# Kernel tuning notes

Hardware: AMD Instinct MI355X
Metric: run time of the kernel (lower is better)

The kernel has to match this reference:

```python
import jax, jax.numpy as jnp
import numpy as np

BZ, N_STEPS, D_IN, D_HID, D_OUT = 4096, 128, 32, 128, 32


def setup_inputs() -> dict:
    key = jax.random.key(0)
    ks = jax.random.split(key, 16)
    g = lambda k, s: jax.random.normal(k, s, dtype=jnp.float32) * 0.05
    return {
        "fcn_latent": g(ks[0], (BZ, D_IN)),
        "encoder_outputs": g(ks[1], (BZ, N_STEPS, D_HID)),
        "att1_w": g(ks[2], (D_IN, 2 * D_IN)),
        "att1_b": g(ks[3], (D_IN,)),
        "att2_w": g(ks[4], (D_HID, 2 * D_HID)),
        "att2_b": g(ks[5], (D_HID,)),
        "gru1_wih": g(ks[6], (3 * D_HID, D_IN)),
        "gru1_whh": g(ks[7], (3 * D_HID, D_HID)),
        "gru1_bih": g(ks[8], (3 * D_HID,)),
        "gru1_bhh": g(ks[9], (3 * D_HID,)),
        "gru2_wih": g(ks[10], (3 * D_HID, D_HID)),
        "gru2_whh": g(ks[11], (3 * D_HID, D_HID)),
        "gru2_bih": g(ks[12], (3 * D_HID,)),
        "gru2_bhh": g(ks[13], (3 * D_HID,)),
        "out_w": g(ks[14], (D_OUT, D_HID)),
        "out_b": g(ks[15], (D_OUT,)),
    }


def _gru_cell(x, h, w_ih, w_hh, b_ih, b_hh):
    # torch.nn.GRUCell math: gates ordered (r, z, n)
    gi = x @ w_ih.T + b_ih
    gh = h @ w_hh.T + b_hh
    i_r, i_z, i_n = jnp.split(gi, 3, axis=-1)
    h_r, h_z, h_n = jnp.split(gh, 3, axis=-1)
    r = jax.nn.sigmoid(i_r + h_r)
    z = jax.nn.sigmoid(i_z + h_z)
    n = jnp.tanh(i_n + r * h_n)
    return (1.0 - z) * n + z * h


def _attend(h, enc_t, w, b):
    # h: (bz, D), enc_t: (bz, d_enc). Faithful to original (mixes batch into contraction).
    scores = h.T @ enc_t                     # (D, d_enc)
    weight = jax.nn.softmax(scores, axis=-1)
    context = (weight @ enc_t.T).T           # (bz, D)
    return jnp.tanh(jnp.concatenate([context, h], axis=1) @ w.T + b)


def reference(fcn_latent, encoder_outputs, att1_w, att1_b, att2_w, att2_b,
              gru1_wih, gru1_whh, gru1_bih, gru1_bhh,
              gru2_wih, gru2_whh, gru2_bih, gru2_bhh, out_w, out_b):
    # step 0: attention over d_input-sized hidden, then GRUCell(d_input -> d_hidden)
    att0 = _attend(fcn_latent, encoder_outputs[:, 0, :], att1_w, att1_b)
    h_rep = jnp.tile(fcn_latent, (1, D_HID // D_IN))          # (bz, d_hidden)
    h = _gru_cell(att0, h_rep, gru1_wih, gru1_whh, gru1_bih, gru1_bhh)

    def step(h, enc_t):
        a = _attend(h, enc_t, att2_w, att2_b)
        h2 = _gru_cell(a, h, gru2_wih, gru2_whh, gru2_bih, gru2_bhh)
        return h2, h2

    enc_rest = jnp.swapaxes(encoder_outputs[:, 1:, :], 0, 1)  # (n_steps-1, bz, d_hidden)
    _, hs_rest = jax.lax.scan(step, h, enc_rest)
    collector = jnp.concatenate([h[:, None, :], jnp.swapaxes(hs_rest, 0, 1)], axis=1)
    reconstruction = collector @ out_w.T + out_b              # (bz, n_steps, d_output)
    return reconstruction
```

## Files before the change

### kernel.cpp

```cpp
#include <hip/hip_runtime.h>
#include <math.h>

#define BZ 4096
#define NT 128
#define DH 128
#define DI 32
#define LDW 132
#define SCR_KS 2116
#define SA 136
#define ST 40

typedef short bf16x8 __attribute__((ext_vector_type(8)));
typedef float f32x4 __attribute__((ext_vector_type(4)));

__device__ __forceinline__ float4 ld4(const float* p) { return *(const float4*)(p); }
__device__ __forceinline__ void st4(float* p, float4 v) { *(float4*)(p) = v; }
__device__ __forceinline__ float dot4(float4 w, float4 a) {
  return w.x*a.x + w.y*a.y + w.z*a.z + w.w*a.w;
}
__device__ __forceinline__ float sigm(float x) { return 1.f / (1.f + expf(-x)); }
__device__ __forceinline__ unsigned short f2b(float x) {
  unsigned u = __float_as_uint(x);
  u += 0x7FFFu + ((u >> 16) & 1u);
  return (unsigned short)(u >> 16);
}

__global__ __launch_bounds__(512) void k_prep(const float* __restrict__ a2w,
                                              const float* __restrict__ wih,
                                              const float* __restrict__ whh,
                                              const float* __restrict__ outw,
                                              unsigned short* __restrict__ wbf) {
  const int idx = blockIdx.x * 512 + threadIdx.x;
  if (idx >= 147456) return;
  const int tile = idx >> 14, pos = idx & 16383;
  float v;
  if (tile == 0)      v = a2w[(pos >> 7) * 256 + (pos & 127)];
  else if (tile == 1) v = a2w[(pos >> 7) * 256 + 128 + (pos & 127)];
  else if (tile == 2) v = wih[pos];
  else if (tile == 3) v = whh[pos];
  else if (tile == 4) v = wih[16384 + pos];
  else if (tile == 5) v = whh[16384 + pos];
  else if (tile == 6) v = wih[32768 + pos];
  else if (tile == 7) v = whh[32768 + pos];
  else                v = (pos < 4096) ? outw[pos] : 0.f;
  wbf[idx] = f2b(v);
}

template<int D>
__global__ __launch_bounds__(512) void k_scores(const float* __restrict__ hsrc,
                                                const float* __restrict__ enc,
                                                int t, float* __restrict__ spart) {
  constexpr int IG = D / 8;
  constexpr int JC = (D == 128) ? 4 : 1;
  constexpr int HS = D + 4;
  __shared__ float hs[64 * HS];
  __shared__ float es[64 * LDW];
  const int p = blockIdx.x, tid = threadIdx.x, b0 = p * 64;
  for (int idx = tid; idx < 64 * (D / 4); idx += 512) {
    const int r = idx / (D / 4), c4 = (idx % (D / 4)) * 4;
    st4(hs + r * HS + c4, ld4(hsrc + (size_t)(b0 + r) * D + c4));
  }
  for (int idx = tid; idx < 64 * 32; idx += 512) {
    const int r = idx >> 5, c4 = (idx & 31) << 2;
    st4(es + r * LDW + c4, ld4(enc + ((size_t)(b0 + r) * NT + t) * DH + c4));
  }
  __syncthreads();
  const int ig = tid % IG, jg = tid / IG;
  const int i0 = ig * 8, j0 = jg * JC;
  float acc[8][JC];
#pragma unroll
  for (int a = 0; a < 8; ++a)
#pragma unroll
    for (int b = 0; b < JC; ++b) acc[a][b] = 0.f;
  for (int b = 0; b < 64; ++b) {
    float4 h0 = ld4(hs + b * HS + i0);
    float4 h1 = ld4(hs + b * HS + i0 + 4);
    float hv[8] = {h0.x, h0.y, h0.z, h0.w, h1.x, h1.y, h1.z, h1.w};
    float ev[JC];
    if (JC == 4) {
      float4 e = ld4(es + b * LDW + j0);
      ev[0] = e.x; ev[1] = e.y; ev[2] = e.z; ev[3] = e.w;
    } else {
      ev[0] = es[b * LDW + j0];
    }
#pragma unroll
    for (int ii = 0; ii < 8; ++ii)
#pragma unroll
      for (int jj = 0; jj < JC; ++jj) acc[ii][jj] += hv[ii] * ev[jj];
  }
#pragma unroll
  for (int ii = 0; ii < 8; ++ii)
#pragma unroll
    for (int jj = 0; jj < JC; ++jj)
      spart[((size_t)p * D + (i0 + ii)) * 128 + j0 + jj] = acc[ii][jj];
}

template<int R, int P>
__global__ __launch_bounds__(128) void k_soft(const float* __restrict__ spart,
                                              float* __restrict__ W,
                                              unsigned short* __restrict__ Wmb) {
  const int r = blockIdx.x, j = threadIdx.x;
  float s = 0.f;
#pragma unroll 8
  for (int p = 0; p < P; ++p) s += spart[((size_t)p * R + r) * 128 + j];
  __shared__ float xm[2], xs[2];
  float m = s;
  for (int o = 1; o < 64; o <<= 1) m = fmaxf(m, __shfl_xor(m, o));
  if ((j & 63) == 0) xm[j >> 6] = m;
  __syncthreads();
  m = fmaxf(xm[0], xm[1]);
  float e = expf(s - m);
  float sum = e;
  for (int o = 1; o < 64; o <<= 1) sum += __shfl_xor(sum, o);
  if ((j & 63) == 0) xs[j >> 6] = sum;
  __syncthreads();
  sum = xs[0] + xs[1];
  const float val = e / sum;
  W[r * 128 + j] = val;
  Wmb[r * 128 + j] = f2b(val);
}

__global__ __launch_bounds__(512) void k_soft2(const float* __restrict__ spart,
                                               unsigned short* __restrict__ Wmb) {
  __shared__ float scr[512];
  __shared__ float xred[4];
  const int r = blockIdx.x, tid = threadIdx.x;
  const int j = tid & 127, pc = tid >> 7;
  float s = 0.f;
#pragma unroll 8
  for (int p = pc * 32; p < (pc + 1) * 32; ++p)
    s += spart[((size_t)p * 128 + r) * 128 + j];
  scr[pc * 128 + j] = s;
  __syncthreads();
  if (tid < 128) {
    const float sv = scr[tid] + scr[128 + tid] + scr[256 + tid] + scr[384 + tid];
    float m = sv;
    for (int o = 1; o < 64; o <<= 1) m = fmaxf(m, __shfl_xor(m, o));
    if ((tid & 63) == 0) xred[tid >> 6] = m;
  }
  __syncthreads();
  if (tid < 128) {
    const float sv = scr[tid] + scr[128 + tid] + scr[256 + tid] + scr[384 + tid];
    const float m = fmaxf(xred[0], xred[1]);
    float ev = expf(sv - m);
    float sum = ev;
    for (int o = 1; o < 64; o <<= 1) sum += __shfl_xor(sum, o);
    if ((tid & 63) == 0) xred[2 + (tid >> 6)] = sum;
  }
  __syncthreads();
  if (tid < 128) {
    const float sv = scr[tid] + scr[128 + tid] + scr[256 + tid] + scr[384 + tid];
    const float m = fmaxf(xred[0], xred[1]);
    const float sum = xred[2] + xred[3];
    Wmb[r * 128 + tid] = f2b(expf(sv - m) / sum);
  }
}

struct WTile { bf16x8 k[4]; };
struct AFrag { bf16x8 k[4]; };

__device__ __forceinline__ void loadW(WTile& wt, const unsigned short* __restrict__ base,
                                      int R, int g) {
#pragma unroll
  for (int ks = 0; ks < 4; ++ks)
    wt.k[ks] = *(const bf16x8*)(base + (size_t)R * 128 + ks * 32 + g * 8);
}
__device__ __forceinline__ void loadA(AFrag& a, const unsigned short* act, int n, int g) {
  const char* ab = (const char*)act + n * (2 * SA) + g * 16;
#pragma unroll
  for (int ks = 0; ks < 4; ++ks) a.k[ks] = *(const bf16x8*)(ab + ks * 64);
}
__device__ __forceinline__ void mmrr(f32x4& acc, const AFrag& a, const WTile& w) {
#pragma unroll
  for (int ks = 0; ks < 4; ++ks)
    acc = __builtin_amdgcn_mfma_f32_16x16x32_bf16(a.k[ks], w.k[ks], acc, 0, 0, 0);
}

__global__ __launch_bounds__(512, 2) void k_step2(
    const float* __restrict__ enc, int t, int do_next,
    const unsigned short* __restrict__ Wmb, const unsigned short* __restrict__ wbf,
    const float* __restrict__ att2b,
    const float* __restrict__ bih, const float* __restrict__ bhh,
    const float* __restrict__ outb,
    float* __restrict__ h, float* __restrict__ out, float* __restrict__ spart) {
  __shared__ __align__(16) unsigned short el[32 * SA], hl[32 * SA];
  __shared__ __align__(16) unsigned short ctxl[32 * SA], al[32 * SA], hnl[32 * SA];
  __shared__ __align__(16) unsigned short hnT[128 * ST], encT[128 * ST];
  const int tid = threadIdx.x, b0 = blockIdx.x * 32;
  const int w = tid >> 6, l = tid & 63;
  const int n = l & 15, g4 = l >> 4;
  const int c = w * 16 + n;
  const f32x4 z4 = {0.f, 0.f, 0.f, 0.f};

  WTile wWm, wA2a, wA2b, wIR, wHR, wIZ, wHZ, wIN, wHN;
  loadW(wWm, Wmb, c, g4);
  loadW(wA2a, wbf + 0 * 16384, c, g4);
  loadW(wA2b, wbf + 1 * 16384, c, g4);
  loadW(wIR,  wbf + 2 * 16384, c, g4);
  loadW(wHR,  wbf + 3 * 16384, c, g4);
  loadW(wIZ,  wbf + 4 * 16384, c, g4);
  loadW(wHZ,  wbf + 5 * 16384, c, g4);
  loadW(wIN,  wbf + 6 * 16384, c, g4);
  loadW(wHN,  wbf + 7 * 16384, c, g4);

  {
    const int r = tid >> 4, c8 = (tid & 15) << 3;
    float4 e0 = ld4(enc + ((size_t)(b0 + r) * NT + t) * DH + c8);
    float4 e1 = ld4(enc + ((size_t)(b0 + r) * NT + t) * DH + c8 + 4);
    float4 h0 = ld4(h + (size_t)(b0 + r) * DH + c8);
    float4 h1 = ld4(h + (size_t)(b0 + r) * DH + c8 + 4);
    unsigned short* ep = el + r * SA + c8;
    ep[0]=f2b(e0.x); ep[1]=f2b(e0.y); ep[2]=f2b(e0.z); ep[3]=f2b(e0.w);
    ep[4]=f2b(e1.x); ep[5]=f2b(e1.y); ep[6]=f2b(e1.z); ep[7]=f2b(e1.w);
    unsigned short* hp = hl + r * SA + c8;
    hp[0]=f2b(h0.x); hp[1]=f2b(h0.y); hp[2]=f2b(h0.z); hp[3]=f2b(h0.w);
    hp[4]=f2b(h1.x); hp[5]=f2b(h1.y); hp[6]=f2b(h1.z); hp[7]=f2b(h1.w);
  }
  if (do_next) {
    const int r = tid & 31, c8 = (tid >> 5) << 3;
    float4 e0 = ld4(enc + ((size_t)(b0 + r) * NT + t + 1) * DH + c8);
    float4 e1 = ld4(enc + ((size_t)(b0 + r) * NT + t + 1) * DH + c8 + 4);
    encT[(c8 + 0) * ST + r] = f2b(e0.x); encT[(c8 + 1) * ST + r] = f2b(e0.y);
    encT[(c8 + 2) * ST + r] = f2b(e0.z); encT[(c8 + 3) * ST + r] = f2b(e0.w);
    encT[(c8 + 4) * ST + r] = f2b(e1.x); encT[(c8 + 5) * ST + r] = f2b(e1.y);
    encT[(c8 + 6) * ST + r] = f2b(e1.z); encT[(c8 + 7) * ST + r] = f2b(e1.w);
  }
  float hprev[2][4];
#pragma unroll
  for (int hh = 0; hh < 2; ++hh)
#pragma unroll
    for (int j = 0; j < 4; ++j)
      hprev[hh][j] = h[(size_t)(b0 + hh * 16 + g4 * 4 + j) * DH + c];
  const float b2c = att2b[c];
  const float bihR = bih[c], bihZ = bih[DH + c], bihN = bih[2 * DH + c];
  const float bhhR = bhh[c], bhhZ = bhh[DH + c], bhhN = bhh[2 * DH + c];
  __syncthreads();

#pragma unroll
  for (int hh = 0; hh < 2; ++hh) {
    AFrag fE;
    loadA(fE, el + hh * 16 * SA, n, g4);
    f32x4 aC = z4;
    mmrr(aC, fE, wWm);
#pragma unroll
    for (int j = 0; j < 4; ++j) ctxl[(hh * 16 + g4 * 4 + j) * SA + c] = f2b(aC[j]);
  }
  __syncthreads();
#pragma unroll
  for (int hh = 0; hh < 2; ++hh) {
    AFrag fC, fH;
    loadA(fC, ctxl + hh * 16 * SA, n, g4);
    loadA(fH, hl + hh * 16 * SA, n, g4);
    f32x4 aA = z4;
    mmrr(aA, fC, wA2a);
    mmrr(aA, fH, wA2b);
#pragma unroll
    for (int j = 0; j < 4; ++j)
      al[(hh * 16 + g4 * 4 + j) * SA + c] = f2b(tanhf(aA[j] + b2c));
  }
  __syncthreads();
  f32x4 aR[2], aZ[2], aIN[2], aHN[2];
#pragma unroll
  for (int hh = 0; hh < 2; ++hh) {
    AFrag fA, fH;
    loadA(fA, al + hh * 16 * SA, n, g4);
    loadA(fH, hl + hh * 16 * SA, n, g4);
    f32x4 tr_ = z4, tz = z4, ti = z4, th = z4;
    mmrr(tr_, fA, wIR); mmrr(tr_, fH, wHR);
    mmrr(tz, fA, wIZ);  mmrr(tz, fH, wHZ);
    mmrr(ti, fA, wIN);  mmrr(th, fH, wHN);
    aR[hh] = tr_; aZ[hh] = tz; aIN[hh] = ti; aHN[hh] = th;
  }
#pragma unroll
  for (int hh = 0; hh < 2; ++hh) {
#pragma unroll
    for (int j = 0; j < 4; ++j) {
      const int row = hh * 16 + g4 * 4 + j;
      const float rg = sigm(aR[hh][j] + bihR + bhhR);
      const float zg = sigm(aZ[hh][j] + bihZ + bhhZ);
      const float ng = tanhf(aIN[hh][j] + bihN + rg * (aHN[hh][j] + bhhN));
      const float hv = (1.f - zg) * ng + zg * hprev[hh][j];
      const unsigned short hb = f2b(hv);
      hnl[row * SA + c] = hb;
      hnT[c * ST + row] = hb;
      h[(size_t)(b0 + row) * DH + c] = hv;
    }
  }
  __syncthreads();
  if (w < 2) {
    WTile wOut;
    loadW(wOut, wbf + 8 * 16384, c, g4);
    const float ob = outb[c];
#pragma unroll
    for (int hh = 0; hh < 2; ++hh) {
      AFrag fO;
      loadA(fO, hnl + hh * 16 * SA, n, g4);
      f32x4 o = z4;
      mmrr(o, fO, wOut);
#pragma unroll
      for (int j = 0; j < 4; ++j)
        out[((size_t)(b0 + hh * 16 + g4 * 4 + j) * NT + t) * DI + c] = o[j] + ob;
    }
  }
  if (do_next) {
    bf16x8 afr = *(const bf16x8*)(hnT + (16 * w + n) * ST + g4 * 8);
    float* spb = spart + ((size_t)blockIdx.x * 128 + 16 * w + g4 * 4) * 128 + n;
#pragma unroll
    for (int nt = 0; nt < 8; ++nt) {
      bf16x8 bfr = *(const bf16x8*)(encT + (16 * nt + n) * ST + g4 * 8);
      f32x4 s = __builtin_amdgcn_mfma_f32_16x16x32_bf16(afr, bfr, z4, 0, 0, 0);
#pragma unroll
      for (int jj = 0; jj < 4; ++jj) spb[(size_t)jj * 128 + 16 * nt] = s[jj];
    }
  }
}

__device__ __forceinline__ void stage128(float* dst, const float* __restrict__ src,
                                         int rows, int srcStride, int tid) {
  const int n4 = rows * 32;
  for (int idx = tid; idx < n4; idx += 512) {
    const int r = idx >> 5, c4 = (idx & 31) << 2;
    st4(dst + r * LDW + c4, ld4(src + (size_t)r * srcStride + c4));
  }
}
template<int ADD>
__device__ __forceinline__ void phase128(float* Wb, const float* act, float* dest, int tid) {
  const int ks = tid & 7, cg_ = (tid >> 3) & 15, r4 = tid >> 7;
  const int rbase = r4 * 4;
  float acc[4][8];
#pragma unroll
  for (int a = 0; a < 4; ++a)
#pragma unroll
    for (int b = 0; b < 8; ++b) acc[a][b] = 0.f;
#pragma unroll
  for (int ch = 0; ch < 4; ++ch) {
    const int k = ks * 4 + ch * 32;
    float4 av[4];
#pragma unroll
    for (int ri = 0; ri < 4; ++ri) av[ri] = ld4(act + (rbase + ri) * LDW + k);
#pragma unroll
    for (int i = 0; i < 8; ++i) {
      float4 wv = ld4(Wb + (cg_ * 8 + i) * LDW + k);
#pragma unroll
      for (int ri = 0; ri < 4; ++ri) acc[ri][i] += dot4(wv, av[ri]);
    }
  }
  __syncthreads();
#pragma unroll
  for (int ri = 0; ri < 4; ++ri) {
    st4(Wb + ks * SCR_KS + (rbase + ri) * LDW + cg_ * 8,
        make_float4(acc[ri][0], acc[ri][1], acc[ri][2], acc[ri][3]));
    st4(Wb + ks * SCR_KS + (rbase + ri) * LDW + cg_ * 8 + 4,
        make_float4(acc[ri][4], acc[ri][5], acc[ri][6], acc[ri][7]));
  }
  __syncthreads();
  const int fr = tid >> 5, fc = (tid & 31) << 2;
  float4 s = make_float4(0.f, 0.f, 0.f, 0.f);
#pragma unroll
  for (int kk = 0; kk < 8; ++kk) {
    float4 v = ld4(Wb + kk * SCR_KS + fr * LDW + fc);
    s.x += v.x; s.y += v.y; s.z += v.z; s.w += v.w;
  }
  float* dp = dest + fr * LDW + fc;
  if (ADD) { float4 o = ld4(dp); s.x += o.x; s.y += o.y; s.z += o.z; s.w += o.w; }
  st4(dp, s);
  __syncthreads();
}
__device__ __forceinline__ void gru_out(float p0, float p1, float p2, float p3,
                                        float bi0, float bi1, float bi2,
                                        float bh0, float bh1, float bh2,
                                        float hv, float* o) {
  const float rg = sigm(p0 + bi0 + bh0);
  const float zg = sigm(p1 + bi1 + bh1);
  const float ng = tanhf(p2 + bi2 + rg * (p3 + bh2));
  *o = (1.f - zg) * ng + zg * hv;
}
__global__ __launch_bounds__(512) void k_main0(
    const float* __restrict__ enc, const float* __restrict__ fcn,
    const float* __restrict__ W0,
    const float* __restrict__ A1, const float* __restrict__ b1,
    const float* __restrict__ wih, const float* __restrict__ whh,
    const float* __restrict__ bih, const float* __restrict__ bhh,
    const float* __restrict__ outw, const float* __restrict__ outb,
    float* __restrict__ h, float* __restrict__ out) {
  __shared__ float Wb[16960];
  __shared__ float el[16 * LDW], hrep[16 * LDW], al[16 * LDW], hn[16 * LDW];
  __shared__ float pre[4][16 * LDW];
  __shared__ float fl[16 * 36];
  const int tid = threadIdx.x, b0 = blockIdx.x * 16;
  {
    const int r = tid >> 5, c4 = (tid & 31) << 2;
    st4(el + r * LDW + c4, ld4(enc + ((size_t)(b0 + r) * NT + 0) * DH + c4));
  }
  {
    const int r = tid >> 5, cc = tid & 31;
    fl[r * 36 + cc] = fcn[(size_t)(b0 + r) * DI + cc];
  }
  __syncthreads();
  {
    const int r = tid >> 5, fc = (tid & 31) << 2;
    st4(hrep + r * LDW + fc, ld4(fl + r * 36 + (fc & 31)));
  }
  stage128(Wb, W0, 32, 128, tid);
  __syncthreads();
  {
    const int r = tid >> 5, q = tid & 31;
    float acc = 0.f;
#pragma unroll 8
    for (int k4 = 0; k4 < 32; ++k4)
      acc += dot4(ld4(Wb + q * LDW + k4 * 4), ld4(el + r * LDW + k4 * 4));
    hn[r * LDW + q] = acc;
  }
  __syncthreads();
  for (int idx = tid; idx < 512; idx += 512) {
    const int r = idx >> 4, c4 = (idx & 15) << 2;
    st4(Wb + r * 68 + c4, ld4(A1 + r * 64 + c4));
  }
  __syncthreads();
  {
    const int r = tid >> 5, i = tid & 31;
    float acc = b1[i];
#pragma unroll
    for (int k4 = 0; k4 < 8; ++k4)
      acc += dot4(ld4(Wb + i * 68 + k4 * 4), ld4(hn + r * LDW + k4 * 4));
#pragma unroll
    for (int k4 = 0; k4 < 8; ++k4)
      acc += dot4(ld4(Wb + i * 68 + 32 + k4 * 4), ld4(fl + r * 36 + k4 * 4));
    al[r * LDW + i] = tanhf(acc);
  }
  __syncthreads();
  for (int idx = tid; idx < 384 * 8; idx += 512) {
    const int r = idx >> 3, c4 = (idx & 7) << 2;
    st4(Wb + r * 36 + c4, ld4(wih + r * 32 + c4));
  }
  __syncthreads();
  {
    const int r = tid >> 5, ccc = tid & 31;
#pragma unroll
    for (int m = 0; m < 12; ++m) {
      const int cc = ccc + 32 * m, g = cc >> 7, col = cc & 127;
      float acc = 0.f;
#pragma unroll
      for (int k4 = 0; k4 < 8; ++k4)
        acc += dot4(ld4(Wb + cc * 36 + k4 * 4), ld4(al + r * LDW + k4 * 4));
      pre[(g == 2) ? 2 : g][r * LDW + col] = acc;
    }
  }
  __syncthreads();
  stage128(Wb, whh, 128, 128, tid);          __syncthreads();
  phase128<1>(Wb, hrep, pre[0], tid);
  stage128(Wb, whh + 16384, 128, 128, tid);  __syncthreads();
  phase128<1>(Wb, hrep, pre[1], tid);
  stage128(Wb, whh + 32768, 128, 128, tid);  __syncthreads();
  phase128<0>(Wb, hrep, pre[3], tid);
  {
    const int fr = tid >> 5, fc = (tid & 31) << 2;
    float4 p0 = ld4(&pre[0][fr * LDW + fc]), p1 = ld4(&pre[1][fr * LDW + fc]);
    float4 p2 = ld4(&pre[2][fr * LDW + fc]), p3 = ld4(&pre[3][fr * LDW + fc]);
    float4 bi0 = ld4(bih + fc), bi1 = ld4(bih + DH + fc), bi2 = ld4(bih + 2 * DH + fc);
    float4 bh0 = ld4(bhh + fc), bh1 = ld4(bhh + DH + fc), bh2 = ld4(bhh + 2 * DH + fc);
    float4 hv = ld4(hrep + fr * LDW + fc);
    float o0, o1, o2, o3;
    gru_out(p0.x, p1.x, p2.x, p3.x, bi0.x, bi1.x, bi2.x, bh0.x, bh1.x, bh2.x, hv.x, &o0);
    gru_out(p0.y, p1.y, p2.y, p3.y, bi0.y, bi1.y, bi2.y, bh0.y, bh1.y, bh2.y, hv.y, &o1);
    gru_out(p0.z, p1.z, p2.z, p3.z, bi0.z, bi1.z, bi2.z, bh0.z, bh1.z, bh2.z, hv.z, &o2);
    gru_out(p0.w, p1.w, p2.w, p3.w, bi0.w, bi1.w, bi2.w, bh0.w, bh1.w, bh2.w, hv.w, &o3);
    float4 hnew = make_float4(o0, o1, o2, o3);
    st4(hn + fr * LDW + fc, hnew);
    st4(h + (size_t)(b0 + fr) * DH + fc, hnew);
  }
  __syncthreads();
  stage128(Wb, outw, 32, 128, tid);
  __syncthreads();
  {
    const int r = tid >> 5, cc = tid & 31;
    float acc = outb[cc];
#pragma unroll 8
    for (int k4 = 0; k4 < 32; ++k4)
      acc += dot4(ld4(Wb + cc * LDW + k4 * 4), ld4(hn + r * LDW + k4 * 4));
    out[((size_t)(b0 + r) * NT + 0) * DI + cc] = acc;
  }
}

extern "C" void kernel_launch(void* const* d_in, const int* in_sizes, int n_in,
                              void* d_out, int out_size, void* d_ws, size_t ws_size,
                              hipStream_t stream) {
  (void)in_sizes; (void)n_in; (void)out_size; (void)ws_size;
  const float* fcn  = (const float*)d_in[0];
  const float* enc  = (const float*)d_in[1];
  const float* a1w  = (const float*)d_in[2];
  const float* a1b  = (const float*)d_in[3];
  const float* a2w  = (const float*)d_in[4];
  const float* a2b  = (const float*)d_in[5];
  const float* w1ih = (const float*)d_in[6];
  const float* w1hh = (const float*)d_in[7];
  const float* b1ih = (const float*)d_in[8];
  const float* b1hh = (const float*)d_in[9];
  const float* w2ih = (const float*)d_in[10];
  const float* w2hh = (const float*)d_in[11];
  const float* b2ih = (const float*)d_in[12];
  const float* b2hh = (const float*)d_in[13];
  const float* outw = (const float*)d_in[14];
  const float* outb = (const float*)d_in[15];
  float* out = (float*)d_out;
  float* ws  = (float*)d_ws;

  float* h     = ws;
  float* spart = ws + 524288;
  float* Wbuf  = ws + 2621440;
  unsigned short* wbf = (unsigned short*)(ws + 2637824);
  unsigned short* Wmb = (unsigned short*)(ws + 2712576);

  k_prep<<<288, 512, 0, stream>>>(a2w, w2ih, w2hh, outw, wbf);

  k_scores<DI><<<64, 512, 0, stream>>>(fcn, enc, 0, spart);
  k_soft<DI, 64><<<DI, 128, 0, stream>>>(spart, Wbuf, Wmb);
  k_main0<<<BZ / 16, 512, 0, stream>>>(enc, fcn, Wbuf, a1w, a1b,
                                       w1ih, w1hh, b1ih, b1hh, outw, outb, h, out);
  k_scores<DH><<<64, 512, 0, stream>>>(h, enc, 1, spart);
  k_soft<DH, 64><<<DH, 128, 0, stream>>>(spart, Wbuf, Wmb);

  for (int t = 1; t < NT; ++t) {
    const int do_next = (t < NT - 1) ? 1 : 0;
    k_step2<<<128, 512, 0, stream>>>(enc, t, do_next, Wmb, wbf, a2b,
                                     b2ih, b2hh, outb, h, out, spart);
    if (do_next)
      k_soft2<<<128, 512, 0, stream>>>(spart, Wmb);
  }
}
```

Before: 3.338 ms.

## Fuse score reduction and softmax into step kernel via atomic accumulation

Drops the separate per-step softmax kernel. Each step block now accumulates its partial attention scores straight into a shared global buffer with atomicAdd, and at the start of the next step recomputes the softmax redundantly per block into a swizzled LDS slot. A ring of four score buffers is rotated, with one buffer zeroed ahead of use, which removes one kernel launch and the partial-score round trip per step. In exchange the atomics contend on a 128x128 buffer, every block repeats the softmax work, and float atomic ordering makes the results nondeterministic.

```diff
diff --git a/kernel.cpp b/kernel.cpp
--- a/kernel.cpp
+++ b/kernel.cpp
@@ -120,40 +120,15 @@
   Wmb[r * 128 + j] = f2b(val);
 }
 
-__global__ __launch_bounds__(512) void k_soft2(const float* __restrict__ spart,
-                                               unsigned short* __restrict__ Wmb) {
-  __shared__ float scr[512];
-  __shared__ float xred[4];
-  const int r = blockIdx.x, tid = threadIdx.x;
-  const int j = tid & 127, pc = tid >> 7;
+__global__ __launch_bounds__(128) void k_sum(const float* __restrict__ spart,
+                                             float* __restrict__ S1,
+                                             float* __restrict__ S2) {
+  const int r = blockIdx.x, j = threadIdx.x;
   float s = 0.f;
 #pragma unroll 8
-  for (int p = pc * 32; p < (pc + 1) * 32; ++p)
-    s += spart[((size_t)p * 128 + r) * 128 + j];
-  scr[pc * 128 + j] = s;
-  __syncthreads();
-  if (tid < 128) {
-    const float sv = scr[tid] + scr[128 + tid] + scr[256 + tid] + scr[384 + tid];
-    float m = sv;
-    for (int o = 1; o < 64; o <<= 1) m = fmaxf(m, __shfl_xor(m, o));
-    if ((tid & 63) == 0) xred[tid >> 6] = m;
-  }
-  __syncthreads();
-  if (tid < 128) {
-    const float sv = scr[tid] + scr[128 + tid] + scr[256 + tid] + scr[384 + tid];
-    const float m = fmaxf(xred[0], xred[1]);
-    float ev = expf(sv - m);
-    float sum = ev;
-    for (int o = 1; o < 64; o <<= 1) sum += __shfl_xor(sum, o);
-    if ((tid & 63) == 0) xred[2 + (tid >> 6)] = sum;
-  }
-  __syncthreads();
-  if (tid < 128) {
-    const float sv = scr[tid] + scr[128 + tid] + scr[256 + tid] + scr[384 + tid];
-    const float m = fmaxf(xred[0], xred[1]);
-    const float sum = xred[2] + xred[3];
-    Wmb[r * 128 + tid] = f2b(expf(sv - m) / sum);
-  }
+  for (int p = 0; p < 64; ++p) s += spart[((size_t)p * 128 + r) * 128 + j];
+  S1[r * 128 + j] = s;
+  S2[r * 128 + j] = 0.f;
 }
 
 struct WTile { bf16x8 k[4]; };
@@ -175,14 +150,28 @@
   for (int ks = 0; ks < 4; ++ks)
     acc = __builtin_amdgcn_mfma_f32_16x16x32_bf16(a.k[ks], w.k[ks], acc, 0, 0, 0);
 }
-
-__global__ __launch_bounds__(512, 2) void k_step2(
+__device__ __forceinline__ void mmls(f32x4& acc, const unsigned short* Wt,
+                                     const unsigned short* act, int R, int n, int g) {
+  const char* ab = (const char*)act + n * (2 * SA) + g * 16;
+  const char* wb = (const char*)Wt;
+  const int sw = (R & 7) << 4;
+#pragma unroll
+  for (int ks = 0; ks < 4; ++ks) {
+    bf16x8 b = *(const bf16x8*)(wb + ((R * 256 + ks * 64 + g * 16) ^ sw));
+    bf16x8 a = *(const bf16x8*)(ab + ks * 64);
+    acc = __builtin_amdgcn_mfma_f32_16x16x32_bf16(a, b, acc, 0, 0, 0);
+  }
+}
+
+__global__ __launch_bounds__(512, 2) void k_step3(
     const float* __restrict__ enc, int t, int do_next,
-    const unsigned short* __restrict__ Wmb, const unsigned short* __restrict__ wbf,
+    const float* __restrict__ Srd, float* __restrict__ Sac, float* __restrict__ Szr,
+    const unsigned short* __restrict__ wbf,
     const float* __restrict__ att2b,
     const float* __restrict__ bih, const float* __restrict__ bhh,
     const float* __restrict__ outb,
-    float* __restrict__ h, float* __restrict__ out, float* __restrict__ spart) {
+    float* __restrict__ h, float* __restrict__ out) {
+  __shared__ __align__(16) unsigned short Wslot[16384];
   __shared__ __align__(16) unsigned short el[32 * SA], hl[32 * SA];
   __shared__ __align__(16) unsigned short ctxl[32 * SA], al[32 * SA], hnl[32 * SA];
   __shared__ __align__(16) unsigned short hnT[128 * ST], encT[128 * ST];
@@ -192,8 +181,67 @@
   const int c = w * 16 + n;
   const f32x4 z4 = {0.f, 0.f, 0.f, 0.f};
 
-  WTile wWm, wA2a, wA2b, wIR, wHR, wIZ, wHZ, wIN, wHN;
-  loadW(wWm, Wmb, c, g4);
+  {
+    const int row = tid >> 2, q = tid & 3;
+    const float* sr = Srd + row * 128 + q * 32;
+    float4 v[8];
+    float mx = -1e30f;
+#pragma unroll
+    for (int i = 0; i < 8; ++i) {
+      v[i] = ld4(sr + 4 * i);
+      mx = fmaxf(mx, fmaxf(fmaxf(v[i].x, v[i].y), fmaxf(v[i].z, v[i].w)));
+    }
+    mx = fmaxf(mx, __shfl_xor(mx, 1));
+    mx = fmaxf(mx, __shfl_xor(mx, 2));
+    float sum = 0.f;
+#pragma unroll
+    for (int i = 0; i < 8; ++i) {
+      v[i].x = expf(v[i].x - mx); v[i].y = expf(v[i].y - mx);
+      v[i].z = expf(v[i].z - mx); v[i].w = expf(v[i].w - mx);
+      sum += (v[i].x + v[i].y) + (v[i].z + v[i].w);
+    }
+    sum += __shfl_xor(sum, 1);
+    sum += __shfl_xor(sum, 2);
+    const float inv = 1.f / sum;
+    char* wb = (char*)Wslot;
+    const int sw = (row & 7) << 4;
+#pragma unroll
+    for (int ch = 0; ch < 4; ++ch) {
+      unsigned short h8[8] = {
+        f2b(v[2*ch].x * inv),   f2b(v[2*ch].y * inv),
+        f2b(v[2*ch].z * inv),   f2b(v[2*ch].w * inv),
+        f2b(v[2*ch+1].x * inv), f2b(v[2*ch+1].y * inv),
+        f2b(v[2*ch+1].z * inv), f2b(v[2*ch+1].w * inv)
+      };
+      *(uint4*)(wb + ((row * 256 + q * 64 + ch * 16) ^ sw)) = *(const uint4*)h8;
+    }
+  }
+
+  {
+    const int r = tid >> 4, c8 = (tid & 15) << 3;
+    float4 e0 = ld4(enc + ((size_t)(b0 + r) * NT + t) * DH + c8);
+    float4 e1 = ld4(enc + ((size_t)(b0 + r) * NT + t) * DH + c8 + 4);
+    float4 h0 = ld4(h + (size_t)(b0 + r) * DH + c8);
+    float4 h1 = ld4(h + (size_t)(b0 + r) * DH + c8 + 4);
+    unsigned short e8[8] = {f2b(e0.x), f2b(e0.y), f2b(e0.z), f2b(e0.w),
+                            f2b(e1.x), f2b(e1.y), f2b(e1.z), f2b(e1.w)};
+    unsigned short h8[8] = {f2b(h0.x), f2b(h0.y), f2b(h0.z), f2b(h0.w),
+                            f2b(h1.x), f2b(h1.y), f2b(h1.z), f2b(h1.w)};
+    *(uint4*)(el + r * SA + c8) = *(const uint4*)e8;
+    *(uint4*)(hl + r * SA + c8) = *(const uint4*)h8;
+  }
+  if (do_next) {
+    const int r = tid & 31, c8 = (tid >> 5) << 3;
+    float4 e0 = ld4(enc + ((size_t)(b0 + r) * NT + t + 1) * DH + c8);
+    float4 e1 = ld4(enc + ((size_t)(b0 + r) * NT + t + 1) * DH + c8 + 4);
+    encT[(c8 + 0) * ST + r] = f2b(e0.x); encT[(c8 + 1) * ST + r] = f2b(e0.y);
+    encT[(c8 + 2) * ST + r] = f2b(e0.z); encT[(c8 + 3) * ST + r] = f2b(e0.w);
+    encT[(c8 + 4) * ST + r] = f2b(e1.x); encT[(c8 + 5) * ST + r] = f2b(e1.y);
+    encT[(c8 + 6) * ST + r] = f2b(e1.z); encT[(c8 + 7) * ST + r] = f2b(e1.w);
+  }
+  if (do_next && tid < 128) Szr[blockIdx.x * 128 + tid] = 0.f;
+
+  WTile wA2a, wA2b, wIR, wHR, wIZ, wHZ, wIN, wHN;
   loadW(wA2a, wbf + 0 * 16384, c, g4);
   loadW(wA2b, wbf + 1 * 16384, c, g4);
   loadW(wIR,  wbf + 2 * 16384, c, g4);
@@ -203,28 +251,6 @@
   loadW(wIN,  wbf + 6 * 16384, c, g4);
   loadW(wHN,  wbf + 7 * 16384, c, g4);
 
-  {
-    const int r = tid >> 4, c8 = (tid & 15) << 3;
-    float4 e0 = ld4(enc + ((size_t)(b0 + r) * NT + t) * DH + c8);
-    float4 e1 = ld4(enc + ((size_t)(b0 + r) * NT + t) * DH + c8 + 4);
-    float4 h0 = ld4(h + (size_t)(b0 + r) * DH + c8);
-    float4 h1 = ld4(h + (size_t)(b0 + r) * DH + c8 + 4);
-    unsigned short* ep = el + r * SA + c8;
-    ep[0]=f2b(e0.x); ep[1]=f2b(e0.y); ep[2]=f2b(e0.z); ep[3]=f2b(e0.w);
-    ep[4]=f2b(e1.x); ep[5]=f2b(e1.y); ep[6]=f2b(e1.z); ep[7]=f2b(e1.w);
-    unsigned short* hp = hl + r * SA + c8;
-    hp[0]=f2b(h0.x); hp[1]=f2b(h0.y); hp[2]=f2b(h0.z); hp[3]=f2b(h0.w);
-    hp[4]=f2b(h1.x); hp[5]=f2b(h1.y); hp[6]=f2b(h1.z); hp[7]=f2b(h1.w);
-  }
-  if (do_next) {
-    const int r = tid & 31, c8 = (tid >> 5) << 3;
-    float4 e0 = ld4(enc + ((size_t)(b0 + r) * NT + t + 1) * DH + c8);
-    float4 e1 = ld4(enc + ((size_t)(b0 + r) * NT + t + 1) * DH + c8 + 4);
-    encT[(c8 + 0) * ST + r] = f2b(e0.x); encT[(c8 + 1) * ST + r] = f2b(e0.y);
-    encT[(c8 + 2) * ST + r] = f2b(e0.z); encT[(c8 + 3) * ST + r] = f2b(e0.w);
-    encT[(c8 + 4) * ST + r] = f2b(e1.x); encT[(c8 + 5) * ST + r] = f2b(e1.y);
-    encT[(c8 + 6) * ST + r] = f2b(e1.z); encT[(c8 + 7) * ST + r] = f2b(e1.w);
-  }
   float hprev[2][4];
 #pragma unroll
   for (int hh = 0; hh < 2; ++hh)
@@ -238,10 +264,8 @@
 
 #pragma unroll
   for (int hh = 0; hh < 2; ++hh) {
-    AFrag fE;
-    loadA(fE, el + hh * 16 * SA, n, g4);
     f32x4 aC = z4;
-    mmrr(aC, fE, wWm);
+    mmls(aC, Wslot, el + hh * 16 * SA, c, n, g4);
 #pragma unroll
     for (int j = 0; j < 4; ++j) ctxl[(hh * 16 + g4 * 4 + j) * SA + c] = f2b(aC[j]);
   }
@@ -304,13 +328,13 @@
   }
   if (do_next) {
     bf16x8 afr = *(const bf16x8*)(hnT + (16 * w + n) * ST + g4 * 8);
-    float* spb = spart + ((size_t)blockIdx.x * 128 + 16 * w + g4 * 4) * 128 + n;
+    float* Sn = Sac + (size_t)(16 * w + g4 * 4) * 128 + n;
 #pragma unroll
     for (int nt = 0; nt < 8; ++nt) {
       bf16x8 bfr = *(const bf16x8*)(encT + (16 * nt + n) * ST + g4 * 8);
       f32x4 s = __builtin_amdgcn_mfma_f32_16x16x32_bf16(afr, bfr, z4, 0, 0, 0);
 #pragma unroll
-      for (int jj = 0; jj < 4; ++jj) spb[(size_t)jj * 128 + 16 * nt] = s[jj];
+      for (int jj = 0; jj < 4; ++jj) atomicAdd(Sn + jj * 128 + nt * 16, s[jj]);
     }
   }
 }
@@ -507,9 +531,10 @@
 
   float* h     = ws;
   float* spart = ws + 524288;
-  float* Wbuf  = ws + 2621440;
-  unsigned short* wbf = (unsigned short*)(ws + 2637824);
-  unsigned short* Wmb = (unsigned short*)(ws + 2712576);
+  float* Wbuf  = ws + 1572864;
+  float* Sbuf  = ws + 1589248;
+  unsigned short* wbf = (unsigned short*)(ws + 1654784);
+  unsigned short* Wmb = (unsigned short*)(ws + 1728512);
 
   k_prep<<<288, 512, 0, stream>>>(a2w, w2ih, w2hh, outw, wbf);
 
@@ -518,13 +543,14 @@
   k_main0<<<BZ / 16, 512, 0, stream>>>(enc, fcn, Wbuf, a1w, a1b,
                                        w1ih, w1hh, b1ih, b1hh, outw, outb, h, out);
   k_scores<DH><<<64, 512, 0, stream>>>(h, enc, 1, spart);
-  k_soft<DH, 64><<<DH, 128, 0, stream>>>(spart, Wbuf, Wmb);
+  k_sum<<<128, 128, 0, stream>>>(spart, Sbuf + 16384, Sbuf + 2 * 16384);
 
   for (int t = 1; t < NT; ++t) {
     const int do_next = (t < NT - 1) ? 1 : 0;
-    k_step2<<<128, 512, 0, stream>>>(enc, t, do_next, Wmb, wbf, a2b,
-                                     b2ih, b2hh, outb, h, out, spart);
-    if (do_next)
-      k_soft2<<<128, 512, 0, stream>>>(spart, Wmb);
-  }
-}
+    const float* Srd = Sbuf + (size_t)(t & 3) * 16384;
+    float* Sac = Sbuf + (size_t)((t + 1) & 3) * 16384;
+    float* Szr = Sbuf + (size_t)((t + 2) & 3) * 16384;
+    k_step3<<<128, 512, 0, stream>>>(enc, t, do_next, Srd, Sac, Szr, wbf, a2b,
+                                     b2ih, b2hh, outb, h, out);
+  }
+}
```

After: 3.242 ms. -2.9%, faster.
